# Kernel optimization log

Hardware: AMD Instinct MI355X
Metric: run time of the kernel (lower is better)

The kernel has to match this reference:

```python
import jax, jax.numpy as jnp
import numpy as np

N_NODES = 50000
N_EDGES = 600000
HIDDEN = 128
HEADS = 8
OUT_CH = HIDDEN // HEADS
NUM_LAYERS = 3
NEG_SLOPE = 0.2   # PyG GATConv default leaky_relu slope
BN_EPS = 1e-5

# Note: dropout is a no-op in eval mode; BatchNorm uses batch statistics
# (training-mode math, the only well-defined choice without running stats).

def setup_inputs() -> dict:
    key = jax.random.key(0)
    ks = jax.random.split(key, 9)
    x = jax.random.normal(ks[0], (N_NODES, HIDDEN), dtype=jnp.float32)
    edge_index = jax.random.randint(ks[1], (2, N_EDGES), 0, N_NODES, dtype=jnp.int64)
    s = 1.0 / np.sqrt(HIDDEN)
    W = jax.random.normal(ks[2], (NUM_LAYERS, HIDDEN, HEADS * OUT_CH), dtype=jnp.float32) * s
    att_src = jax.random.normal(ks[3], (NUM_LAYERS, HEADS, OUT_CH), dtype=jnp.float32) * s
    att_dst = jax.random.normal(ks[4], (NUM_LAYERS, HEADS, OUT_CH), dtype=jnp.float32) * s
    bias = jnp.zeros((NUM_LAYERS, HIDDEN), dtype=jnp.float32)
    gamma = jnp.ones((NUM_LAYERS, HIDDEN), dtype=jnp.float32)
    beta = jnp.zeros((NUM_LAYERS, HIDDEN), dtype=jnp.float32)
    return {"x": x, "edge_index": edge_index, "W": W, "att_src": att_src,
            "att_dst": att_dst, "bias": bias, "gamma": gamma, "beta": beta}


def _gat_layer(x, src, dst, W, a_src, a_dst, b):
    n = x.shape[0]
    h = (x @ W).reshape(n, HEADS, OUT_CH)              # [N,H,C]
    alpha_s = jnp.einsum('nhc,hc->nh', h, a_src)        # [N,H]
    alpha_d = jnp.einsum('nhc,hc->nh', h, a_dst)
    e = jax.nn.leaky_relu(alpha_s[src] + alpha_d[dst], NEG_SLOPE)  # [E,H]
    # segment softmax over incoming edges of each destination node
    m = jax.ops.segment_max(e, dst, num_segments=n)     # [N,H]
    e = jnp.exp(e - m[dst])
    z = jax.ops.segment_sum(e, dst, num_segments=n)
    alpha = e / (z[dst] + 1e-16)                        # [E,H]
    msg = h[src] * alpha[:, :, None]                    # [E,H,C]
    out = jax.ops.segment_sum(msg, dst, num_segments=n) # [N,H,C]
    return out.reshape(n, HEADS * OUT_CH) + b


def _batchnorm(x, gamma, beta):
    mu = x.mean(axis=0)
    var = x.var(axis=0)
    return (x - mu) * jax.lax.rsqrt(var + BN_EPS) * gamma + beta


def reference(x, edge_index, W, att_src, att_dst, bias, gamma, beta):
    src, dst = edge_index[0], edge_index[1]
    for l in range(NUM_LAYERS):
        x = _gat_layer(x, src, dst, W[l], att_src[l], att_dst[l], bias[l])
        x = _batchnorm(x, gamma[l], beta[l])
        x = jax.nn.elu(x)
    return x
```

## Files before the change

kernel.cpp:

```cpp
#include <hip/hip_runtime.h>
#include <hip/hip_bf16.h>

#define N_NODES 50000
#define N_EDGES 600000
#define HID 128
#define HEADS 8
#define OUTC 16
#define NEG_SLOPE 0.2f
#define BN_EPS 1e-5f

typedef __attribute__((ext_vector_type(8))) short short8;
typedef __attribute__((ext_vector_type(4))) float floatx4;

__device__ __forceinline__ float bf_lo(unsigned int v) { return __uint_as_float(v << 16); }
__device__ __forceinline__ float bf_hi(unsigned int v) { return __uint_as_float(v & 0xffff0000u); }

__device__ __forceinline__ short f2bfs(float v) {
    __hip_bfloat16 b = __float2bfloat16(v);
    return *reinterpret_cast<short*>(&b);
}

__global__ void k_hist(const int* __restrict__ dst, int* __restrict__ deg, int e) {
    int i = blockIdx.x * 256 + threadIdx.x;
    if (i < e) atomicAdd(&deg[dst[i]], 1);
}

__global__ void k_scan1(const int* __restrict__ deg, int* __restrict__ incl,
                        int* __restrict__ partials, int n) {
    __shared__ int sh[512];
    int i = blockIdx.x * 512 + threadIdx.x;
    int v = (i < n) ? deg[i] : 0;
    sh[threadIdx.x] = v;
    __syncthreads();
    for (int off = 1; off < 512; off <<= 1) {
        int t = (threadIdx.x >= off) ? sh[threadIdx.x - off] : 0;
        __syncthreads();
        sh[threadIdx.x] += t;
        __syncthreads();
    }
    if (i < n) incl[i] = sh[threadIdx.x];
    if (threadIdx.x == 511) partials[blockIdx.x] = sh[511];
}

__global__ void k_scan2(int* __restrict__ partials, int nb) {
    __shared__ int sh[128];
    int v = (threadIdx.x < nb) ? partials[threadIdx.x] : 0;
    sh[threadIdx.x] = v;
    __syncthreads();
    for (int off = 1; off < 128; off <<= 1) {
        int t = (threadIdx.x >= off) ? sh[threadIdx.x - off] : 0;
        __syncthreads();
        sh[threadIdx.x] += t;
        __syncthreads();
    }
    if (threadIdx.x < nb) partials[threadIdx.x] = sh[threadIdx.x] - v;
}

__global__ void k_scan3(const int* __restrict__ deg, const int* __restrict__ incl,
                        const int* __restrict__ partials, int* __restrict__ row_ptr,
                        int* __restrict__ cursor, int n, int e_total) {
    int i = blockIdx.x * 512 + threadIdx.x;
    if (i < n) {
        int rp = incl[i] - deg[i] + partials[blockIdx.x];
        row_ptr[i] = rp;
        cursor[i] = rp;
    }
    if (i == 0) row_ptr[n] = e_total;
}

__global__ void k_scatter(const int* __restrict__ src, const int* __restrict__ dst,
                          int* __restrict__ cursor, int* __restrict__ col_src, int e) {
    int i = blockIdx.x * 256 + threadIdx.x;
    if (i < e) {
        int d = dst[i];
        int p = atomicAdd(&cursor[d], 1);
        col_src[p] = src[i];
    }
}

__global__ void k_wt(const float* __restrict__ W, __hip_bfloat16* __restrict__ Wt) {
    int i = blockIdx.x * 256 + threadIdx.x;
    if (i >= 3 * 16384) return;
    int l = i >> 14, r = i & 16383, n = r >> 7, k = r & 127;
    Wt[i] = __float2bfloat16(W[l * 16384 + k * 128 + n]);
}

__global__ void k_wa(const float* __restrict__ W, const float* __restrict__ asrc,
                     const float* __restrict__ adst, __hip_bfloat16* __restrict__ WAT) {
    int i = blockIdx.x * 256 + threadIdx.x;
    if (i >= 3 * 2048) return;
    int l = i >> 11, r = i & 2047, j = r >> 7, k = r & 127;
    const float* att = (j < 8) ? (asrc + l * 128 + j * 16) : (adst + l * 128 + (j - 8) * 16);
    const float* Wrow = W + l * 16384 + k * 128 + (j & 7) * 16;
    float sum = 0.f;
#pragma unroll
    for (int c = 0; c < 16; c++) sum += Wrow[c] * att[c];
    WAT[i] = __float2bfloat16(sum);
}

__global__ __launch_bounds__(256) void k_gemm(const float* __restrict__ Xf,
                                              const float* __restrict__ stats,
                                              const float* __restrict__ gamma,
                                              const float* __restrict__ beta,
                                              const __hip_bfloat16* __restrict__ Wt,
                                              const __hip_bfloat16* __restrict__ WAT,
                                              __hip_bfloat16* __restrict__ Hb,
                                              float* __restrict__ AS, float* __restrict__ AD,
                                              int n_nodes, int apply_bn) {
    __shared__ float s_scale[128], s_shift[128];
    if (apply_bn && threadIdx.x < 128) {
        int c = threadIdx.x;
        float invN = 1.0f / (float)N_NODES;
        float mu = stats[c] * invN;
        float var = stats[128 + c] * invN - mu * mu;
        float sc = rsqrtf(var + BN_EPS) * gamma[c];
        s_scale[c] = sc;
        s_shift[c] = beta[c] - mu * sc;
    }
    __syncthreads();

    int wave = threadIdx.x >> 6, lane = threadIdx.x & 63;
    int row0 = blockIdx.x * 64 + wave * 16;
    int m_lane = lane & 15, kq = lane >> 4;
    floatx4 acc[8] = {};
    floatx4 acc_a = {};
    const short* Ws = (const short*)Wt;
    const short* Was = (const short*)WAT;
    int r = row0 + m_lane;
    int rr = (r < n_nodes) ? r : 0;
    for (int c = 0; c < 4; c++) {
        const float4* xp = (const float4*)(Xf + (size_t)rr * 128 + c * 32 + kq * 8);
        float4 v0 = xp[0], v1 = xp[1];
        float vals[8] = {v0.x, v0.y, v0.z, v0.w, v1.x, v1.y, v1.z, v1.w};
        short8 a;
        if (apply_bn) {
            int ch0 = c * 32 + kq * 8;
#pragma unroll
            for (int j = 0; j < 8; j++) {
                float val = fmaf(vals[j], s_scale[ch0 + j], s_shift[ch0 + j]);
                val = (val > 0.f) ? val : (__expf(val) - 1.0f);
                a[j] = f2bfs(val);
            }
        } else {
#pragma unroll
            for (int j = 0; j < 8; j++)
                a[j] = f2bfs(vals[j]);
        }
        for (int t = 0; t < 8; t++) {
            short8 b = *(const short8*)(Ws + (t * 16 + m_lane) * 128 + c * 32 + kq * 8);
            acc[t] = __builtin_amdgcn_mfma_f32_16x16x32_bf16(a, b, acc[t], 0, 0, 0);
        }
        short8 bwa = *(const short8*)(Was + m_lane * 128 + c * 32 + kq * 8);
        acc_a = __builtin_amdgcn_mfma_f32_16x16x32_bf16(a, bwa, acc_a, 0, 0, 0);
    }
#pragma unroll
    for (int reg = 0; reg < 4; reg++) {
        int row = row0 + kq * 4 + reg;
        if (row >= n_nodes) continue;
#pragma unroll
        for (int t = 0; t < 8; t++)
            Hb[(size_t)row * 128 + t * 16 + m_lane] = __float2bfloat16(acc[t][reg]);
        float av = acc_a[reg];
        if (m_lane < 8) AS[row * 8 + m_lane] = av;
        else            AD[row * 8 + (m_lane - 8)] = av;
    }
}

__global__ __launch_bounds__(256) void k_agg(const int* __restrict__ RP,
                                             const int* __restrict__ COL,
                                             const float* __restrict__ AS,
                                             const float* __restrict__ AD,
                                             const __hip_bfloat16* __restrict__ Hb,
                                             const float* __restrict__ bias,
                                             float* __restrict__ out, int n_nodes) {
    int wave = threadIdx.x >> 6, lane = threadIdx.x & 63;
    int n = blockIdx.x * 4 + wave;
    if (n >= n_nodes) return;
    int e_l = lane >> 3, h = lane & 7;
    int p0 = RP[n], p1 = RP[n + 1];
    float ad = AD[n * 8 + h];
    float z = 0.f;
    float acc[16];
#pragma unroll
    for (int c = 0; c < 16; c++) acc[c] = 0.f;
    const unsigned short* Hu = (const unsigned short*)Hb;
    for (int p = p0 + e_l; p < p1; p += 8) {
        int s = COL[p];
        float e = AS[s * 8 + h] + ad;
        e = (e > 0.f) ? e : NEG_SLOPE * e;
        float w = __expf(e);
        z += w;
        const uint4* hp = (const uint4*)(Hu + (size_t)s * 128 + h * 16);
        uint4 h0 = hp[0];
        uint4 h1 = hp[1];
        unsigned int ww[8] = {h0.x, h0.y, h0.z, h0.w, h1.x, h1.y, h1.z, h1.w};
#pragma unroll
        for (int j = 0; j < 8; j++) {
            acc[2 * j]     += w * bf_lo(ww[j]);
            acc[2 * j + 1] += w * bf_hi(ww[j]);
        }
    }
#pragma unroll
    for (int off = 8; off < 64; off <<= 1) {
        z += __shfl_xor(z, off, 64);
#pragma unroll
        for (int c = 0; c < 16; c++) acc[c] += __shfl_xor(acc[c], off, 64);
    }
    if (e_l == 0) {
        float inv = 1.0f / (z + 1e-16f);
        float4* op = (float4*)(out + (size_t)n * 128 + h * 16);
        const float* bp = bias + h * 16;
#pragma unroll
        for (int q = 0; q < 4; q++) {
            op[q] = make_float4(acc[4 * q]     * inv + bp[4 * q],
                                acc[4 * q + 1] * inv + bp[4 * q + 1],
                                acc[4 * q + 2] * inv + bp[4 * q + 2],
                                acc[4 * q + 3] * inv + bp[4 * q + 3]);
        }
    }
}

__global__ __launch_bounds__(256) void k_bnstats(const float* __restrict__ x,
                                                 float* __restrict__ partials, int n_nodes) {
    int tid = threadIdx.x;
    int c4 = tid & 31, sub = tid >> 5;
    int g = blockIdx.x * 8 + sub;
    float sx = 0.f, sy = 0.f, sz = 0.f, sw = 0.f;
    float qx = 0.f, qy = 0.f, qz = 0.f, qw = 0.f;
    for (int n = g; n < n_nodes; n += 2048) {
        float4 v = *(const float4*)(x + (size_t)n * 128 + c4 * 4);
        sx += v.x; sy += v.y; sz += v.z; sw += v.w;
        qx += v.x * v.x; qy += v.y * v.y; qz += v.z * v.z; qw += v.w * v.w;
    }
    __shared__ float ssum[8][128];
    __shared__ float ssq[8][128];
    int c = c4 * 4;
    ssum[sub][c] = sx; ssum[sub][c + 1] = sy; ssum[sub][c + 2] = sz; ssum[sub][c + 3] = sw;
    ssq[sub][c] = qx;  ssq[sub][c + 1] = qy;  ssq[sub][c + 2] = qz;  ssq[sub][c + 3] = qw;
    __syncthreads();
    float total = 0.f;
    if (tid < 128) {
#pragma unroll
        for (int k = 0; k < 8; k++) total += ssum[k][tid];
    } else {
        int cc = tid - 128;
#pragma unroll
        for (int k = 0; k < 8; k++) total += ssq[k][cc];
    }
    partials[blockIdx.x * 256 + tid] = total;
}

__global__ void k_bnreduce(const float* __restrict__ partials, float* __restrict__ stats) {
    int t = threadIdx.x;
    float s = 0.f;
#pragma unroll 8
    for (int b = 0; b < 256; b++) s += partials[b * 256 + t];
    stats[t] = s;
}

__global__ void k_bnapply(const float* __restrict__ x, const float* __restrict__ stats,
                          const float* __restrict__ gamma, const float* __restrict__ beta,
                          float* __restrict__ outf, int n_nodes) {
    int i = blockIdx.x * 256 + threadIdx.x;
    if (i >= n_nodes * 32) return;
    float4 v = *(const float4*)(x + (size_t)i * 4);
    int c0 = (i * 4) & 127;
    float r[4] = {v.x, v.y, v.z, v.w};
    float invN = 1.0f / (float)N_NODES;
#pragma unroll
    for (int j = 0; j < 4; j++) {
        int c = c0 + j;
        float mu = stats[c] * invN;
        float var = stats[128 + c] * invN - mu * mu;
        float sc = rsqrtf(var + BN_EPS) * gamma[c];
        float val = (r[j] - mu) * sc + beta[c];
        val = (val > 0.f) ? val : (__expf(val) - 1.0f);
        r[j] = val;
    }
    *(float4*)(outf + (size_t)i * 4) = make_float4(r[0], r[1], r[2], r[3]);
}

extern "C" void kernel_launch(void* const* d_in, const int* in_sizes, int n_in,
                              void* d_out, int out_size, void* d_ws, size_t ws_size,
                              hipStream_t stream) {
    const float* x_in   = (const float*)d_in[0];
    const int*   eidx   = (const int*)d_in[1];
    const float* W      = (const float*)d_in[2];
    const float* attsrc = (const float*)d_in[3];
    const float* attdst = (const float*)d_in[4];
    const float* bias   = (const float*)d_in[5];
    const float* gamma  = (const float*)d_in[6];
    const float* beta   = (const float*)d_in[7];
    float* out = (float*)d_out;

    const int N = N_NODES, E = N_EDGES;
    const int* src = eidx;
    const int* dst = eidx + E;

    char* base = (char*)d_ws;
    size_t off = 0;
    auto carve = [&](size_t bytes) -> char* {
        char* p = base + off;
        off += (bytes + 255) & ~(size_t)255;
        return p;
    };
    __hip_bfloat16* Hb  = (__hip_bfloat16*)carve((size_t)N * HID * 2);
    float*          XN  = (float*)carve((size_t)N * HID * 4);
    float*          AS  = (float*)carve((size_t)N * HEADS * 4);
    float*          AD  = (float*)carve((size_t)N * HEADS * 4);
    __hip_bfloat16* WT  = (__hip_bfloat16*)carve((size_t)3 * HID * HID * 2);
    __hip_bfloat16* WAT = (__hip_bfloat16*)carve((size_t)3 * 16 * HID * 2);
    float*          STA = (float*)carve(3 * 256 * 4);
    float*          PAR = (float*)carve(256 * 256 * 4);
    int*            DEG = (int*)carve((size_t)N * 4);
    int*            INC = (int*)carve((size_t)N * 4);
    int*            RP  = (int*)carve((size_t)(N + 1) * 4);
    int*            CUR = (int*)carve((size_t)N * 4);
    int*            PRT = (int*)carve(1024 * 4);
    int*            COL = (int*)carve((size_t)E * 4);

    const int NB_E  = (E + 255) / 256;
    const int NB_SC = (N + 511) / 512;

    (void)hipMemsetAsync(DEG, 0, (size_t)N * 4, stream);

    k_hist<<<NB_E, 256, 0, stream>>>(dst, DEG, E);
    k_scan1<<<NB_SC, 512, 0, stream>>>(DEG, INC, PRT, N);
    k_scan2<<<1, 128, 0, stream>>>(PRT, NB_SC);
    k_scan3<<<NB_SC, 512, 0, stream>>>(DEG, INC, PRT, RP, CUR, N, E);
    k_scatter<<<NB_E, 256, 0, stream>>>(src, dst, CUR, COL, E);

    k_wt<<<(3 * 16384 + 255) / 256, 256, 0, stream>>>(W, WT);
    k_wa<<<(3 * 2048 + 255) / 256, 256, 0, stream>>>(W, attsrc, attdst, WAT);

    for (int l = 0; l < 3; l++) {
        const float* Xf = (l == 0) ? x_in : XN;
        const float* st = (l == 0) ? nullptr : (STA + (l - 1) * 256);
        const float* gm = gamma + (l - 1) * 128;
        const float* bt = beta + (l - 1) * 128;
        k_gemm<<<(N + 63) / 64, 256, 0, stream>>>(Xf, st, gm, bt,
                                                  WT + l * 16384, WAT + l * 2048,
                                                  Hb, AS, AD, N, (l == 0) ? 0 : 1);
        k_agg<<<(N + 3) / 4, 256, 0, stream>>>(RP, COL, AS, AD, Hb, bias + l * 128, XN, N);
        k_bnstats<<<256, 256, 0, stream>>>(XN, PAR, N);
        k_bnreduce<<<1, 256, 0, stream>>>(PAR, STA + l * 256);
    }
    k_bnapply<<<(N * 32 + 255) / 256, 256, 0, stream>>>(XN, STA + 2 * 256,
                                                        gamma + 2 * 128, beta + 2 * 128, out, N);
}
```

Baseline: 387.0 us.

## Merge setup kernels, fold BN reduce into stats, drop bias cancelled by BatchNorm

New measurement: 544.3 us. 1.41x slower.

```diff
diff --git a/kernel.cpp b/kernel.cpp
--- a/kernel.cpp
+++ b/kernel.cpp
@@ -25,47 +25,47 @@
     if (i < e) atomicAdd(&deg[dst[i]], 1);
 }
 
-__global__ void k_scan1(const int* __restrict__ deg, int* __restrict__ incl,
-                        int* __restrict__ partials, int n) {
-    __shared__ int sh[512];
-    int i = blockIdx.x * 512 + threadIdx.x;
-    int v = (i < n) ? deg[i] : 0;
-    sh[threadIdx.x] = v;
-    __syncthreads();
-    for (int off = 1; off < 512; off <<= 1) {
-        int t = (threadIdx.x >= off) ? sh[threadIdx.x - off] : 0;
-        __syncthreads();
-        sh[threadIdx.x] += t;
-        __syncthreads();
-    }
-    if (i < n) incl[i] = sh[threadIdx.x];
-    if (threadIdx.x == 511) partials[blockIdx.x] = sh[511];
-}
-
-__global__ void k_scan2(int* __restrict__ partials, int nb) {
-    __shared__ int sh[128];
-    int v = (threadIdx.x < nb) ? partials[threadIdx.x] : 0;
-    sh[threadIdx.x] = v;
-    __syncthreads();
-    for (int off = 1; off < 128; off <<= 1) {
-        int t = (threadIdx.x >= off) ? sh[threadIdx.x - off] : 0;
-        __syncthreads();
-        sh[threadIdx.x] += t;
-        __syncthreads();
-    }
-    if (threadIdx.x < nb) partials[threadIdx.x] = sh[threadIdx.x] - v;
-}
-
-__global__ void k_scan3(const int* __restrict__ deg, const int* __restrict__ incl,
-                        const int* __restrict__ partials, int* __restrict__ row_ptr,
-                        int* __restrict__ cursor, int n, int e_total) {
-    int i = blockIdx.x * 512 + threadIdx.x;
-    if (i < n) {
-        int rp = incl[i] - deg[i] + partials[blockIdx.x];
-        row_ptr[i] = rp;
-        cursor[i] = rp;
-    }
-    if (i == 0) row_ptr[n] = e_total;
+__global__ __launch_bounds__(1024) void k_scan(const int* __restrict__ deg,
+                                               int* __restrict__ RP, int* __restrict__ CUR,
+                                               int n, int e_total) {
+    const int CH = (N_NODES + 1023) / 1024;
+    int t = threadIdx.x;
+    int base = t * CH;
+    int sum = 0;
+    for (int j = 0; j < CH; j++) {
+        int i = base + j;
+        if (i < n) sum += deg[i];
+    }
+    __shared__ int wsum[16];
+    int lane = t & 63, wid = t >> 6;
+    int v = sum;
+#pragma unroll
+    for (int off = 1; off < 64; off <<= 1) {
+        int u = __shfl_up(v, off, 64);
+        if (lane >= off) v += u;
+    }
+    if (lane == 63) wsum[wid] = v;
+    __syncthreads();
+    if (wid == 0 && lane < 16) {
+        int wv = wsum[lane];
+#pragma unroll
+        for (int off = 1; off < 16; off <<= 1) {
+            int wu = __shfl_up(wv, off, 16);
+            if (lane >= off) wv += wu;
+        }
+        wsum[lane] = wv;
+    }
+    __syncthreads();
+    int run = (wid > 0 ? wsum[wid - 1] : 0) + (v - sum);
+    for (int j = 0; j < CH; j++) {
+        int i = base + j;
+        if (i < n) {
+            RP[i] = run;
+            CUR[i] = run;
+            run += deg[i];
+        }
+    }
+    if (t == 0) RP[n] = e_total;
 }
 
 __global__ void k_scatter(const int* __restrict__ src, const int* __restrict__ dst,
@@ -78,24 +78,23 @@
     }
 }
 
-__global__ void k_wt(const float* __restrict__ W, __hip_bfloat16* __restrict__ Wt) {
+__global__ void k_wtwa(const float* __restrict__ W, const float* __restrict__ asrc,
+                       const float* __restrict__ adst, __hip_bfloat16* __restrict__ Wt,
+                       __hip_bfloat16* __restrict__ WAT) {
     int i = blockIdx.x * 256 + threadIdx.x;
-    if (i >= 3 * 16384) return;
-    int l = i >> 14, r = i & 16383, n = r >> 7, k = r & 127;
-    Wt[i] = __float2bfloat16(W[l * 16384 + k * 128 + n]);
-}
-
-__global__ void k_wa(const float* __restrict__ W, const float* __restrict__ asrc,
-                     const float* __restrict__ adst, __hip_bfloat16* __restrict__ WAT) {
-    int i = blockIdx.x * 256 + threadIdx.x;
-    if (i >= 3 * 2048) return;
-    int l = i >> 11, r = i & 2047, j = r >> 7, k = r & 127;
-    const float* att = (j < 8) ? (asrc + l * 128 + j * 16) : (adst + l * 128 + (j - 8) * 16);
-    const float* Wrow = W + l * 16384 + k * 128 + (j & 7) * 16;
-    float sum = 0.f;
-#pragma unroll
-    for (int c = 0; c < 16; c++) sum += Wrow[c] * att[c];
-    WAT[i] = __float2bfloat16(sum);
+    if (i < 3 * 16384) {
+        int l = i >> 14, r = i & 16383, n = r >> 7, k = r & 127;
+        Wt[i] = __float2bfloat16(W[l * 16384 + k * 128 + n]);
+    } else {
+        int q = i - 3 * 16384;
+        int l = q >> 11, r = q & 2047, j = r >> 7, k = r & 127;
+        const float* att = (j < 8) ? (asrc + l * 128 + j * 16) : (adst + l * 128 + (j - 8) * 16);
+        const float* Wrow = W + l * 16384 + k * 128 + (j & 7) * 16;
+        float sum = 0.f;
+#pragma unroll
+        for (int c = 0; c < 16; c++) sum += Wrow[c] * att[c];
+        WAT[q] = __float2bfloat16(sum);
+    }
 }
 
 __global__ __launch_bounds__(256) void k_gemm(const float* __restrict__ Xf,
@@ -171,7 +170,6 @@
                                              const float* __restrict__ AS,
                                              const float* __restrict__ AD,
                                              const __hip_bfloat16* __restrict__ Hb,
-                                             const float* __restrict__ bias,
                                              float* __restrict__ out, int n_nodes) {
     int wave = threadIdx.x >> 6, lane = threadIdx.x & 63;
     int n = blockIdx.x * 4 + wave;
@@ -209,19 +207,18 @@
     if (e_l == 0) {
         float inv = 1.0f / (z + 1e-16f);
         float4* op = (float4*)(out + (size_t)n * 128 + h * 16);
-        const float* bp = bias + h * 16;
 #pragma unroll
         for (int q = 0; q < 4; q++) {
-            op[q] = make_float4(acc[4 * q]     * inv + bp[4 * q],
-                                acc[4 * q + 1] * inv + bp[4 * q + 1],
-                                acc[4 * q + 2] * inv + bp[4 * q + 2],
-                                acc[4 * q + 3] * inv + bp[4 * q + 3]);
+            op[q] = make_float4(acc[4 * q] * inv, acc[4 * q + 1] * inv,
+                                acc[4 * q + 2] * inv, acc[4 * q + 3] * inv);
         }
     }
 }
 
 __global__ __launch_bounds__(256) void k_bnstats(const float* __restrict__ x,
-                                                 float* __restrict__ partials, int n_nodes) {
+                                                 float* __restrict__ partials,
+                                                 float* __restrict__ stats,
+                                                 int* __restrict__ counter, int n_nodes) {
     int tid = threadIdx.x;
     int c4 = tid & 31, sub = tid >> 5;
     int g = blockIdx.x * 8 + sub;
@@ -248,14 +245,15 @@
         for (int k = 0; k < 8; k++) total += ssq[k][cc];
     }
     partials[blockIdx.x * 256 + tid] = total;
-}
-
-__global__ void k_bnreduce(const float* __restrict__ partials, float* __restrict__ stats) {
-    int t = threadIdx.x;
-    float s = 0.f;
-#pragma unroll 8
-    for (int b = 0; b < 256; b++) s += partials[b * 256 + t];
-    stats[t] = s;
+    __threadfence();
+    __shared__ int s_last;
+    if (tid == 0) s_last = (atomicAdd(counter, 1) == 255) ? 1 : 0;
+    __syncthreads();
+    if (s_last) {
+        float s = 0.f;
+        for (int b = 0; b < 256; b++) s += partials[b * 256 + tid];
+        stats[tid] = s;
+    }
 }
 
 __global__ void k_bnapply(const float* __restrict__ x, const float* __restrict__ stats,
@@ -288,7 +286,6 @@
     const float* W      = (const float*)d_in[2];
     const float* attsrc = (const float*)d_in[3];
     const float* attdst = (const float*)d_in[4];
-    const float* bias   = (const float*)d_in[5];
     const float* gamma  = (const float*)d_in[6];
     const float* beta   = (const float*)d_in[7];
     float* out = (float*)d_out;
@@ -312,26 +309,21 @@
     __hip_bfloat16* WAT = (__hip_bfloat16*)carve((size_t)3 * 16 * HID * 2);
     float*          STA = (float*)carve(3 * 256 * 4);
     float*          PAR = (float*)carve(256 * 256 * 4);
+    int*            CNT = (int*)carve(256);
     int*            DEG = (int*)carve((size_t)N * 4);
-    int*            INC = (int*)carve((size_t)N * 4);
     int*            RP  = (int*)carve((size_t)(N + 1) * 4);
     int*            CUR = (int*)carve((size_t)N * 4);
-    int*            PRT = (int*)carve(1024 * 4);
     int*            COL = (int*)carve((size_t)E * 4);
 
-    const int NB_E  = (E + 255) / 256;
-    const int NB_SC = (N + 511) / 512;
-
-    (void)hipMemsetAsync(DEG, 0, (size_t)N * 4, stream);
+    const int NB_E = (E + 255) / 256;
+
+    (void)hipMemsetAsync(CNT, 0, 256 + (size_t)N * 4, stream);
 
     k_hist<<<NB_E, 256, 0, stream>>>(dst, DEG, E);
-    k_scan1<<<NB_SC, 512, 0, stream>>>(DEG, INC, PRT, N);
-    k_scan2<<<1, 128, 0, stream>>>(PRT, NB_SC);
-    k_scan3<<<NB_SC, 512, 0, stream>>>(DEG, INC, PRT, RP, CUR, N, E);
+    k_scan<<<1, 1024, 0, stream>>>(DEG, RP, CUR, N, E);
     k_scatter<<<NB_E, 256, 0, stream>>>(src, dst, CUR, COL, E);
 
-    k_wt<<<(3 * 16384 + 255) / 256, 256, 0, stream>>>(W, WT);
-    k_wa<<<(3 * 2048 + 255) / 256, 256, 0, stream>>>(W, attsrc, attdst, WAT);
+    k_wtwa<<<216, 256, 0, stream>>>(W, attsrc, attdst, WT, WAT);
 
     for (int l = 0; l < 3; l++) {
         const float* Xf = (l == 0) ? x_in : XN;
@@ -341,9 +333,8 @@
         k_gemm<<<(N + 63) / 64, 256, 0, stream>>>(Xf, st, gm, bt,
                                                   WT + l * 16384, WAT + l * 2048,
                                                   Hb, AS, AD, N, (l == 0) ? 0 : 1);
-        k_agg<<<(N + 3) / 4, 256, 0, stream>>>(RP, COL, AS, AD, Hb, bias + l * 128, XN, N);
-        k_bnstats<<<256, 256, 0, stream>>>(XN, PAR, N);
-        k_bnreduce<<<1, 256, 0, stream>>>(PAR, STA + l * 256);
+        k_agg<<<(N + 3) / 4, 256, 0, stream>>>(RP, COL, AS, AD, Hb, XN, N);
+        k_bnstats<<<256, 256, 0, stream>>>(XN, PAR, STA + l * 256, CNT + l, N);
     }
     k_bnapply<<<(N * 32 + 255) / 256, 256, 0, stream>>>(XN, STA + 2 * 256,
                                                         gamma + 2 * 128, beta + 2 * 128, out, N);
```
